# Performance work log

Hardware: AMD Instinct MI355X
Metric: run time of the kernel (lower is better)

Reference implementation:

```python
import jax, jax.numpy as jnp
import numpy as np

N = 100000
E = 1600000
F_IN = 128
F_HID = 128


def gcn_conv(x, src, dst, deg_inv_sqrt, W, b, n_nodes):
    # x: [N, Fin] -> [N, Fout]; symmetric-normalized aggregation with self-loops
    h = x @ W  # [N, Fout]
    norm = deg_inv_sqrt[src] * deg_inv_sqrt[dst]  # [E+N] (self-loops appended)
    msgs = h[src] * norm[:, None]  # [E+N, Fout]
    out = jax.ops.segment_sum(msgs, dst, num_segments=n_nodes)
    return out + b


def setup_inputs() -> dict:
    key = jax.random.key(0)
    k = jax.random.split(key, 8)
    x = jax.random.normal(k[0], (N, F_IN), dtype=jnp.float32)
    edge_index = jax.random.randint(k[1], (2, E), 0, N, dtype=jnp.int32)
    s = 1.0 / np.sqrt(F_IN)
    W1 = jax.random.uniform(k[2], (F_IN, F_HID), jnp.float32, -s, s)
    b1 = jnp.zeros((F_HID,), jnp.float32)
    s2 = 1.0 / np.sqrt(F_HID)
    W2 = jax.random.uniform(k[3], (F_HID, F_HID), jnp.float32, -s2, s2)
    b2 = jnp.zeros((F_HID,), jnp.float32)
    W3 = jax.random.uniform(k[4], (F_HID, 1), jnp.float32, -s2, s2)
    b3 = jnp.zeros((1,), jnp.float32)
    return {"x": x, "edge_index": edge_index, "W1": W1, "b1": b1,
            "W2": W2, "b2": b2, "W3": W3, "b3": b3}


def reference(x, edge_index, W1, b1, W2, b2, W3, b3):
    n = x.shape[0]
    loops = jnp.arange(n, dtype=edge_index.dtype)
    src = jnp.concatenate([edge_index[0], loops])  # add self-loops
    dst = jnp.concatenate([edge_index[1], loops])
    deg = jax.ops.segment_sum(jnp.ones_like(dst, dtype=x.dtype), dst, num_segments=n)
    deg_inv_sqrt = jnp.where(deg > 0, jax.lax.rsqrt(deg), 0.0)

    h = gcn_conv(x, src, dst, deg_inv_sqrt, W1, b1, n)
    h = jax.nn.relu(h)  # dropout is identity at inference
    h = gcn_conv(h, src, dst, deg_inv_sqrt, W2, b2, n)
    h = jax.nn.relu(h)
    h = gcn_conv(h, src, dst, deg_inv_sqrt, W3, b3, n)
    return jax.nn.sigmoid(h)  # [N, 1]
```

## Files before the change

kernel.cpp:

```cpp
#include <hip/hip_runtime.h>
#include <cstdint>
#include <cstddef>

#define NN 100000
#define NE 1600000
#define FD 128
#define NXCD 8
#define RNODES ((NN + NXCD - 1) / NXCD)
#define CAP 208192

typedef int vi4 __attribute__((ext_vector_type(4)));
typedef __attribute__((ext_vector_type(8))) short bf16x8;
typedef __attribute__((ext_vector_type(4))) float f32x4;

__device__ __forceinline__ float bf_lo(uint32_t u) { return __uint_as_float(u << 16); }
__device__ __forceinline__ float bf_hi(uint32_t u) { return __uint_as_float(u & 0xffff0000u); }
__device__ __forceinline__ uint32_t bf_pack(float a, float b) {
    uint32_t ua = __float_as_uint(a), ub = __float_as_uint(b);
    ua += 0x7fffu + ((ua >> 16) & 1u);
    ub += 0x7fffu + ((ub >> 16) & 1u);
    return (ua >> 16) | (ub & 0xffff0000u);
}
__device__ __forceinline__ unsigned short bf1(float a) {
    uint32_t u = __float_as_uint(a);
    u += 0x7fffu + ((u >> 16) & 1u);
    return (unsigned short)(u >> 16);
}

__global__ __launch_bounds__(256) void k_part(const int* __restrict__ src,
                                              const int* __restrict__ dst,
                                              uint32_t* __restrict__ bkt,
                                              int* __restrict__ bcnt, int e) {
    __shared__ int scnt[8];
    __shared__ int sbase[8];
    if (threadIdx.x < 8) scnt[threadIdx.x] = 0;
    __syncthreads();
    const int base = blockIdx.x * 1024 + threadIdx.x * 4;
    const bool valid = base < e;
    int b_[4]; int r_[4]; uint32_t u_[4];
    if (valid) {
        vi4 d4 = __builtin_nontemporal_load((const vi4*)(dst + base));
        vi4 s4 = __builtin_nontemporal_load((const vi4*)(src + base));
        #pragma unroll
        for (int j = 0; j < 4; ++j) {
            int d = d4[j], s = s4[j];
            int b = d / RNODES;
            b_[j] = b;
            u_[j] = ((uint32_t)(d - b * RNODES) << 17) | (uint32_t)s;
            r_[j] = atomicAdd(&scnt[b], 1);
        }
    }
    __syncthreads();
    if (threadIdx.x < 8)
        sbase[threadIdx.x] = atomicAdd(&bcnt[threadIdx.x], scnt[threadIdx.x]);
    __syncthreads();
    if (valid) {
        #pragma unroll
        for (int j = 0; j < 4; ++j) {
            int b = b_[j];
            bkt[(size_t)b * CAP + sbase[b] + r_[j]] = u_[j];
        }
    }
}

__global__ __launch_bounds__(256) void k_hist2(const uint32_t* __restrict__ bkt,
                                               const int* __restrict__ bcnt,
                                               int* __restrict__ cnt) {
    const int xcd  = blockIdx.x & 7;
    const int blk  = blockIdx.x >> 3;
    const int nblk = (int)(gridDim.x >> 3);
    const int m = bcnt[xcd];
    const uint32_t* B = bkt + (size_t)xcd * CAP;
    const int lo = xcd * RNODES;
    for (int i = blk * 256 + threadIdx.x; i < m; i += nblk * 256)
        atomicAdd(&cnt[lo + (int)(B[i] >> 17)], 1);
}

__global__ __launch_bounds__(1024) void k_scan1(const int* __restrict__ cnt,
                                                int* __restrict__ excl,
                                                int* __restrict__ bsum, int n) {
    __shared__ int sh[1024];
    int i = blockIdx.x * 1024 + threadIdx.x;
    int v = (i < n) ? cnt[i] : 0;
    sh[threadIdx.x] = v;
    __syncthreads();
    for (int off = 1; off < 1024; off <<= 1) {
        int t = (threadIdx.x >= off) ? sh[threadIdx.x - off] : 0;
        __syncthreads();
        sh[threadIdx.x] += t;
        __syncthreads();
    }
    if (i < n) excl[i] = sh[threadIdx.x] - v;
    if (threadIdx.x == 1023) bsum[blockIdx.x] = sh[1023];
}

__global__ void k_scan2(int* __restrict__ bsum, int nb) {
    __shared__ int sh[128];
    int t = threadIdx.x;
    int v = (t < nb) ? bsum[t] : 0;
    sh[t] = v;
    __syncthreads();
    for (int off = 1; off < 128; off <<= 1) {
        int u = (t >= off) ? sh[t - off] : 0;
        __syncthreads();
        sh[t] += u;
        __syncthreads();
    }
    if (t < nb) bsum[t] = sh[t] - v;
}

__global__ void k_scan3(int* __restrict__ excl, const int* __restrict__ bsum,
                        int* __restrict__ cursor, const int* __restrict__ cnt,
                        float* __restrict__ dis, int n, int e) {
    int i = blockIdx.x * blockDim.x + threadIdx.x;
    if (i < n) {
        int v = excl[i] + bsum[i >> 10];
        excl[i] = v;
        cursor[i] = v;
        dis[i] = rsqrtf((float)(cnt[i] + 1));
    }
    if (i == 0) excl[n] = e;
}

__global__ __launch_bounds__(256) void k_fill2(const uint32_t* __restrict__ bkt,
                                               const int* __restrict__ bcnt,
                                               int* __restrict__ cursor,
                                               uint2* __restrict__ colw,
                                               const float* __restrict__ dis) {
    const int xcd  = blockIdx.x & 7;
    const int blk  = blockIdx.x >> 3;
    const int nblk = (int)(gridDim.x >> 3);
    const int m = bcnt[xcd];
    const uint32_t* B = bkt + (size_t)xcd * CAP;
    const int lo = xcd * RNODES;
    for (int i = blk * 256 + threadIdx.x; i < m; i += nblk * 256) {
        uint32_t u = B[i];
        int s = (int)(u & 0x1FFFFu);
        int d = lo + (int)(u >> 17);
        int pos = atomicAdd(&cursor[d], 1);
        uint2 cw;
        cw.x = (uint32_t)s;
        cw.y = __float_as_uint(dis[s] * dis[d]);
        colw[pos] = cw;
    }
}

template <typename TIN>
__global__ __launch_bounds__(256) void k_gemm(const TIN* __restrict__ X,
                                              const float* __restrict__ W,
                                              unsigned short* __restrict__ H, int n) {
    __shared__ unsigned short Wl[128][136];
    const int t = threadIdx.x;
    #pragma unroll
    for (int c = 0; c < 16; ++c) {
        int idx4 = (c * 256 + t) * 4;
        int k  = idx4 >> 7;
        int nn = idx4 & 127;
        float4 v = *(const float4*)(W + idx4);
        Wl[nn + 0][k] = bf1(v.x);
        Wl[nn + 1][k] = bf1(v.y);
        Wl[nn + 2][k] = bf1(v.z);
        Wl[nn + 3][k] = bf1(v.w);
    }
    __syncthreads();

    const int wave = t >> 6, lane = t & 63;
    const int row0 = blockIdx.x * 64 + wave * 16;
    if (row0 >= n) return;
    const int arow = row0 + (lane & 15);
    const int kb8  = (lane >> 4) * 8;

    bf16x8 a[4];
    if constexpr (sizeof(TIN) == 4) {
        const float* Xf = (const float*)X;
        #pragma unroll
        for (int kt = 0; kt < 4; ++kt) {
            const float* p = Xf + (size_t)arow * FD + kt * 32 + kb8;
            float4 u0 = *(const float4*)p;
            float4 u1 = *(const float4*)(p + 4);
            bf16x8 f;
            f[0] = (short)bf1(u0.x); f[1] = (short)bf1(u0.y);
            f[2] = (short)bf1(u0.z); f[3] = (short)bf1(u0.w);
            f[4] = (short)bf1(u1.x); f[5] = (short)bf1(u1.y);
            f[6] = (short)bf1(u1.z); f[7] = (short)bf1(u1.w);
            a[kt] = f;
        }
    } else {
        const unsigned short* Xb = (const unsigned short*)X;
        #pragma unroll
        for (int kt = 0; kt < 4; ++kt)
            a[kt] = *(const bf16x8*)(Xb + (size_t)arow * FD + kt * 32 + kb8);
    }

    const int ccol  = lane & 15;
    const int crow0 = row0 + (lane >> 4) * 4;
    #pragma unroll
    for (int nt = 0; nt < 8; ++nt) {
        f32x4 acc = {0.f, 0.f, 0.f, 0.f};
        const int bcol = nt * 16 + (lane & 15);
        #pragma unroll
        for (int kt = 0; kt < 4; ++kt) {
            bf16x8 b = *(const bf16x8*)&Wl[bcol][kt * 32 + kb8];
            acc = __builtin_amdgcn_mfma_f32_16x16x32_bf16(a[kt], b, acc, 0, 0, 0);
        }
        #pragma unroll
        for (int j = 0; j < 4; ++j)
            H[(size_t)(crow0 + j) * FD + nt * 16 + ccol] = bf1(acc[j]);
    }
}

template <int MODE>
__global__ __launch_bounds__(256) void k_agg(const unsigned short* __restrict__ h,
                                             const float* __restrict__ dis,
                                             const int* __restrict__ rp,
                                             const uint2* __restrict__ colw,
                                             const float* __restrict__ bias,
                                             const float* __restrict__ W3,
                                             unsigned short* __restrict__ out,
                                             float* __restrict__ outf, int n) {
    const uint32_t* h32 = (const uint32_t*)h;
    int wid  = (int)((blockIdx.x * (size_t)blockDim.x + threadIdx.x) >> 6);
    int lane = threadIdx.x & 63;
    int w2 = __builtin_amdgcn_readfirstlane(wid);
    int i0 = 2 * w2;
    if (i0 >= n) return;
    int i1 = i0 + 1;
    const bool has1 = (i1 < n);

    const int e00 = rp[i0];
    const int e01 = rp[i0 + 1];
    const int e11 = has1 ? rp[i0 + 2] : e01;

    float di0 = dis[i0];
    float di1 = has1 ? dis[i1] : 0.f;
    float2 acc0, acc1;
    {
        uint32_t su0 = h32[(size_t)i0 * 64 + lane];
        float q0 = di0 * di0;
        acc0.x = bf_lo(su0) * q0; acc0.y = bf_hi(su0) * q0;
        if (has1) {
            uint32_t su1 = h32[(size_t)i1 * 64 + lane];
            float q1 = di1 * di1;
            acc1.x = bf_lo(su1) * q1; acc1.y = bf_hi(su1) * q1;
        } else { acc1.x = acc1.y = 0.f; }
    }

    const int ng0 = (e01 - e00 + 15) >> 4;
    const int ng1 = (e11 - e01 + 15) >> 4;
    const int ng  = ng0 > ng1 ? ng0 : ng1;

    for (int g = 0; g < ng; ++g) {
        const bool do0 = (g < ng0), do1 = (g < ng1);
        int s0[16], s1[16];
        float w0_[16], w1_[16];
        uint32_t v0[16], v1[16];
        if (do0) {
            const int jb = e00 + g * 16;
            if (jb + 16 <= e01) {
                #pragma unroll
                for (int q = 0; q < 16; ++q) {
                    uint2 cw = colw[jb + q];
                    s0[q] = (int)cw.x; w0_[q] = __uint_as_float(cw.y);
                }
            } else {
                #pragma unroll
                for (int q = 0; q < 16; ++q) {
                    int idx = jb + q;
                    int c   = idx < e01 ? idx : e01 - 1;
                    uint2 cw = colw[c];
                    s0[q]  = (int)cw.x;
                    w0_[q] = idx < e01 ? __uint_as_float(cw.y) : 0.f;
                }
            }
        }
        if (do1) {
            const int jb = e01 + g * 16;
            if (jb + 16 <= e11) {
                #pragma unroll
                for (int q = 0; q < 16; ++q) {
                    uint2 cw = colw[jb + q];
                    s1[q] = (int)cw.x; w1_[q] = __uint_as_float(cw.y);
                }
            } else {
                #pragma unroll
                for (int q = 0; q < 16; ++q) {
                    int idx = jb + q;
                    int c   = idx < e11 ? idx : e11 - 1;
                    uint2 cw = colw[c];
                    s1[q]  = (int)cw.x;
                    w1_[q] = idx < e11 ? __uint_as_float(cw.y) : 0.f;
                }
            }
        }
        if (do0) {
            #pragma unroll
            for (int q = 0; q < 16; ++q)
                v0[q] = h32[(size_t)s0[q] * 64 + lane];
        }
        if (do1) {
            #pragma unroll
            for (int q = 0; q < 16; ++q)
                v1[q] = h32[(size_t)s1[q] * 64 + lane];
        }
        if (do0) {
            #pragma unroll
            for (int q = 0; q < 16; ++q) {
                acc0.x = fmaf(w0_[q], bf_lo(v0[q]), acc0.x);
                acc0.y = fmaf(w0_[q], bf_hi(v0[q]), acc0.y);
            }
        }
        if (do1) {
            #pragma unroll
            for (int q = 0; q < 16; ++q) {
                acc1.x = fmaf(w1_[q], bf_lo(v1[q]), acc1.x);
                acc1.y = fmaf(w1_[q], bf_hi(v1[q]), acc1.y);
            }
        }
    }

    float2 b = ((const float2*)bias)[lane];
    acc0.x = fmaxf(acc0.x + b.x, 0.f);
    acc0.y = fmaxf(acc0.y + b.y, 0.f);
    acc1.x = fmaxf(acc1.x + b.x, 0.f);
    acc1.y = fmaxf(acc1.y + b.y, 0.f);

    if (MODE == 0) {
        ((uint32_t*)out)[(size_t)i0 * 64 + lane] = bf_pack(acc0.x, acc0.y);
        if (has1)
            ((uint32_t*)out)[(size_t)i1 * 64 + lane] = bf_pack(acc1.x, acc1.y);
    } else {
        float2 w3 = ((const float2*)W3)[lane];
        float d0 = acc0.x * w3.x + acc0.y * w3.y;
        float d1 = acc1.x * w3.x + acc1.y * w3.y;
        #pragma unroll
        for (int off = 32; off; off >>= 1) {
            d0 += __shfl_xor(d0, off);
            d1 += __shfl_xor(d1, off);
        }
        if (lane == 0) {
            outf[i0] = d0;
            if (has1) outf[i1] = d1;
        }
    }
}

__global__ __launch_bounds__(256) void k_agg1(const float* __restrict__ h3,
                                              const float* __restrict__ dis,
                                              const int* __restrict__ rp,
                                              const uint2* __restrict__ colw,
                                              const float* __restrict__ b3,
                                              float* __restrict__ out, int n) {
    int i    = (int)((blockIdx.x * (size_t)blockDim.x + threadIdx.x) >> 6);
    int lane = threadIdx.x & 63;
    if (i >= n) return;
    float di  = dis[i];
    float acc = (lane == 0) ? di * di * h3[i] : 0.f;
    const int e0 = rp[i], e1 = rp[i + 1];
    for (int base = e0 + lane; base < e1; base += 64) {
        uint2 cw = colw[base];
        acc = fmaf(__uint_as_float(cw.y), h3[(int)cw.x], acc);
    }
    #pragma unroll
    for (int off = 32; off; off >>= 1) acc += __shfl_xor(acc, off);
    if (lane == 0) {
        float v = acc + b3[0];
        out[i] = 1.f / (1.f + expf(-v));
    }
}

static inline size_t alg(size_t x) { return (x + 255) & ~(size_t)255; }

extern "C" void kernel_launch(void* const* d_in, const int* in_sizes, int n_in,
                              void* d_out, int out_size, void* d_ws, size_t ws_size,
                              hipStream_t stream) {
    const float* x   = (const float*)d_in[0];
    const int*   ei  = (const int*)d_in[1];
    const float* W1  = (const float*)d_in[2];
    const float* b1  = (const float*)d_in[3];
    const float* W2  = (const float*)d_in[4];
    const float* b2  = (const float*)d_in[5];
    const float* W3  = (const float*)d_in[6];
    const float* b3  = (const float*)d_in[7];
    float*       out = (float*)d_out;

    const int n = NN, e = NE;
    const int* src = ei;
    const int* dst = ei + e;

    char* w = (char*)d_ws;
    float* dis    = (float*)w;  w += alg((size_t)n * 4);
    int*   cnt    = (int*)w;    w += alg((size_t)n * 4);
    int*   bcnt   = (int*)w;    w += alg((size_t)8 * 4);
    int*   rp     = (int*)w;    w += alg((size_t)(n + 1) * 4);
    int*   cursor = (int*)w;    w += alg((size_t)n * 4);
    int*   bsum   = (int*)w;    w += alg((size_t)128 * 4);
    uint32_t* bkt = (uint32_t*)w; w += alg((size_t)NXCD * CAP * 4);
    uint2* colw   = (uint2*)w;  w += alg((size_t)e * 8);
    unsigned short* bufA = (unsigned short*)w; w += alg((size_t)n * FD * 2);
    unsigned short* bufB = (unsigned short*)w; w += alg((size_t)n * FD * 2);
    float* h3     = (float*)w;  w += alg((size_t)n * 4);

    hipMemsetAsync(cnt, 0, (size_t)n * 4, stream);
    hipMemsetAsync(bcnt, 0, 8 * 4, stream);

    const int B = 256;
    const int gN = (n + B - 1) / B;
    const int nScan = (n + 1023) / 1024;
    const int nChunk = (e + 1023) / 1024;

    k_part<<<nChunk, B, 0, stream>>>(src, dst, bkt, bcnt, e);
    k_hist2<<<2048, B, 0, stream>>>(bkt, bcnt, cnt);
    k_scan1<<<nScan, 1024, 0, stream>>>(cnt, rp, bsum, n);
    k_scan2<<<1, 128, 0, stream>>>(bsum, nScan);
    k_scan3<<<gN, B, 0, stream>>>(rp, bsum, cursor, cnt, dis, n, e);
    k_fill2<<<2048, B, 0, stream>>>(bkt, bcnt, cursor, colw, dis);

    const int gGemm = (n + 63) / 64;
    const int nWave2  = (n + 1) / 2;
    const int gWave2  = (nWave2 * 64 + B - 1) / B;
    const int gWave   = (n * 64 + B - 1) / B;

    k_gemm<float><<<gGemm, B, 0, stream>>>(x, W1, bufA, n);
    k_agg<0><<<gWave2, B, 0, stream>>>(bufA, dis, rp, colw, b1, W3, bufB, h3, n);
    k_gemm<unsigned short><<<gGemm, B, 0, stream>>>(bufB, W2, bufA, n);
    k_agg<1><<<gWave2, B, 0, stream>>>(bufA, dis, rp, colw, b2, W3, bufB, h3, n);
    k_agg1<<<gWave, B, 0, stream>>>(h3, dis, rp, colw, b3, out, n);
}
```

Before: 486.4 us.

## Process four nodes per wave in aggregation and pre-convert weights to bf16

The aggregation kernel now has each 64-lane wave handle four destination nodes instead of two. This issues up to 64 independent gathered row loads per group iteration, raising memory-level parallelism on the edge gather. A small new kernel converts W1 and W2 to bf16 once, so each GEMM block loads bf16 weights instead of converting fp32 per block. The cost is much higher register pressure from the 4x16 index, weight and value arrays, which may lower occupancy or cause spills. Work imbalance also grows, since each wave loops until its highest-degree node is done.

```diff
diff --git a/kernel.cpp b/kernel.cpp
--- a/kernel.cpp
+++ b/kernel.cpp
@@ -25,6 +25,23 @@
     uint32_t u = __float_as_uint(a);
     u += 0x7fffu + ((u >> 16) & 1u);
     return (unsigned short)(u >> 16);
+}
+
+__global__ __launch_bounds__(256) void k_wcvt(const float* __restrict__ W1,
+                                              const float* __restrict__ W2,
+                                              unsigned short* __restrict__ Wb1,
+                                              unsigned short* __restrict__ Wb2) {
+    int idx4 = (blockIdx.x * 256 + threadIdx.x) * 4;
+    if (idx4 < FD * FD) {
+        float4 a = *(const float4*)(W1 + idx4);
+        ushort4 o;
+        o.x = bf1(a.x); o.y = bf1(a.y); o.z = bf1(a.z); o.w = bf1(a.w);
+        *(ushort4*)(Wb1 + idx4) = o;
+        float4 b = *(const float4*)(W2 + idx4);
+        ushort4 p;
+        p.x = bf1(b.x); p.y = bf1(b.y); p.z = bf1(b.z); p.w = bf1(b.w);
+        *(ushort4*)(Wb2 + idx4) = p;
+    }
 }
 
 __global__ __launch_bounds__(256) void k_part(const int* __restrict__ src,
@@ -147,20 +164,21 @@
 
 template <typename TIN>
 __global__ __launch_bounds__(256) void k_gemm(const TIN* __restrict__ X,
-                                              const float* __restrict__ W,
+                                              const unsigned short* __restrict__ Wb,
                                               unsigned short* __restrict__ H, int n) {
     __shared__ unsigned short Wl[128][136];
     const int t = threadIdx.x;
     #pragma unroll
-    for (int c = 0; c < 16; ++c) {
-        int idx4 = (c * 256 + t) * 4;
-        int k  = idx4 >> 7;
-        int nn = idx4 & 127;
-        float4 v = *(const float4*)(W + idx4);
-        Wl[nn + 0][k] = bf1(v.x);
-        Wl[nn + 1][k] = bf1(v.y);
-        Wl[nn + 2][k] = bf1(v.z);
-        Wl[nn + 3][k] = bf1(v.w);
+    for (int c = 0; c < 8; ++c) {
+        int idx8 = (c * 256 + t) * 8;
+        int k  = idx8 >> 7;
+        int nn = idx8 & 127;
+        ushort4 v0 = *(const ushort4*)(Wb + idx8);
+        ushort4 v1 = *(const ushort4*)(Wb + idx8 + 4);
+        Wl[nn + 0][k] = v0.x; Wl[nn + 1][k] = v0.y;
+        Wl[nn + 2][k] = v0.z; Wl[nn + 3][k] = v0.w;
+        Wl[nn + 4][k] = v1.x; Wl[nn + 5][k] = v1.y;
+        Wl[nn + 6][k] = v1.z; Wl[nn + 7][k] = v1.w;
     }
     __syncthreads();
 
@@ -221,125 +239,111 @@
     const uint32_t* h32 = (const uint32_t*)h;
     int wid  = (int)((blockIdx.x * (size_t)blockDim.x + threadIdx.x) >> 6);
     int lane = threadIdx.x & 63;
-    int w2 = __builtin_amdgcn_readfirstlane(wid);
-    int i0 = 2 * w2;
+    int w4 = __builtin_amdgcn_readfirstlane(wid);
+    int i0 = 4 * w4;
     if (i0 >= n) return;
-    int i1 = i0 + 1;
-    const bool has1 = (i1 < n);
-
-    const int e00 = rp[i0];
-    const int e01 = rp[i0 + 1];
-    const int e11 = has1 ? rp[i0 + 2] : e01;
-
-    float di0 = dis[i0];
-    float di1 = has1 ? dis[i1] : 0.f;
-    float2 acc0, acc1;
-    {
-        uint32_t su0 = h32[(size_t)i0 * 64 + lane];
-        float q0 = di0 * di0;
-        acc0.x = bf_lo(su0) * q0; acc0.y = bf_hi(su0) * q0;
-        if (has1) {
-            uint32_t su1 = h32[(size_t)i1 * 64 + lane];
-            float q1 = di1 * di1;
-            acc1.x = bf_lo(su1) * q1; acc1.y = bf_hi(su1) * q1;
-        } else { acc1.x = acc1.y = 0.f; }
-    }
-
-    const int ng0 = (e01 - e00 + 15) >> 4;
-    const int ng1 = (e11 - e01 + 15) >> 4;
-    const int ng  = ng0 > ng1 ? ng0 : ng1;
-
-    for (int g = 0; g < ng; ++g) {
-        const bool do0 = (g < ng0), do1 = (g < ng1);
-        int s0[16], s1[16];
-        float w0_[16], w1_[16];
-        uint32_t v0[16], v1[16];
-        if (do0) {
-            const int jb = e00 + g * 16;
-            if (jb + 16 <= e01) {
+
+    int eb[5];
+    #pragma unroll
+    for (int k = 0; k < 5; ++k) {
+        int idx = i0 + k;
+        eb[k] = rp[idx < n ? idx : n];
+    }
+
+    float2 acc[4];
+    #pragma unroll
+    for (int k = 0; k < 4; ++k) {
+        int i = i0 + k;
+        if (i < n) {
+            float di = dis[i];
+            float q  = di * di;
+            uint32_t su = h32[(size_t)i * 64 + lane];
+            acc[k].x = bf_lo(su) * q;
+            acc[k].y = bf_hi(su) * q;
+        } else { acc[k].x = 0.f; acc[k].y = 0.f; }
+    }
+
+    int ng[4], ngmax = 0;
+    #pragma unroll
+    for (int k = 0; k < 4; ++k) {
+        ng[k] = (eb[k + 1] - eb[k] + 15) >> 4;
+        ngmax = ng[k] > ngmax ? ng[k] : ngmax;
+    }
+
+    for (int g = 0; g < ngmax; ++g) {
+        int s[4][16]; float wt[4][16]; uint32_t v[4][16];
+        #pragma unroll
+        for (int k = 0; k < 4; ++k) {
+            if (g < ng[k]) {
+                const int jb = eb[k] + g * 16;
+                const int ee = eb[k + 1];
+                if (jb + 16 <= ee) {
+                    #pragma unroll
+                    for (int q = 0; q < 16; ++q) {
+                        uint2 cw = colw[jb + q];
+                        s[k][q] = (int)cw.x; wt[k][q] = __uint_as_float(cw.y);
+                    }
+                } else {
+                    #pragma unroll
+                    for (int q = 0; q < 16; ++q) {
+                        int idx = jb + q;
+                        int c   = idx < ee ? idx : ee - 1;
+                        uint2 cw = colw[c];
+                        s[k][q]  = (int)cw.x;
+                        wt[k][q] = idx < ee ? __uint_as_float(cw.y) : 0.f;
+                    }
+                }
+            }
+        }
+        #pragma unroll
+        for (int k = 0; k < 4; ++k) {
+            if (g < ng[k]) {
+                #pragma unroll
+                for (int q = 0; q < 16; ++q)
+                    v[k][q] = h32[(size_t)s[k][q] * 64 + lane];
+            }
+        }
+        #pragma unroll
+        for (int k = 0; k < 4; ++k) {
+            if (g < ng[k]) {
                 #pragma unroll
                 for (int q = 0; q < 16; ++q) {
-                    uint2 cw = colw[jb + q];
-                    s0[q] = (int)cw.x; w0_[q] = __uint_as_float(cw.y);
-                }
-            } else {
-                #pragma unroll
-                for (int q = 0; q < 16; ++q) {
-                    int idx = jb + q;
-                    int c   = idx < e01 ? idx : e01 - 1;
-                    uint2 cw = colw[c];
-                    s0[q]  = (int)cw.x;
-                    w0_[q] = idx < e01 ? __uint_as_float(cw.y) : 0.f;
+                    acc[k].x = fmaf(wt[k][q], bf_lo(v[k][q]), acc[k].x);
+                    acc[k].y = fmaf(wt[k][q], bf_hi(v[k][q]), acc[k].y);
                 }
             }
         }
-        if (do1) {
-            const int jb = e01 + g * 16;
-            if (jb + 16 <= e11) {
-                #pragma unroll
-                for (int q = 0; q < 16; ++q) {
-                    uint2 cw = colw[jb + q];
-                    s1[q] = (int)cw.x; w1_[q] = __uint_as_float(cw.y);
-                }
-            } else {
-                #pragma unroll
-                for (int q = 0; q < 16; ++q) {
-                    int idx = jb + q;
-                    int c   = idx < e11 ? idx : e11 - 1;
-                    uint2 cw = colw[c];
-                    s1[q]  = (int)cw.x;
-                    w1_[q] = idx < e11 ? __uint_as_float(cw.y) : 0.f;
-                }
-            }
-        }
-        if (do0) {
-            #pragma unroll
-            for (int q = 0; q < 16; ++q)
-                v0[q] = h32[(size_t)s0[q] * 64 + lane];
-        }
-        if (do1) {
-            #pragma unroll
-            for (int q = 0; q < 16; ++q)
-                v1[q] = h32[(size_t)s1[q] * 64 + lane];
-        }
-        if (do0) {
-            #pragma unroll
-            for (int q = 0; q < 16; ++q) {
-                acc0.x = fmaf(w0_[q], bf_lo(v0[q]), acc0.x);
-                acc0.y = fmaf(w0_[q], bf_hi(v0[q]), acc0.y);
-            }
-        }
-        if (do1) {
-            #pragma unroll
-            for (int q = 0; q < 16; ++q) {
-                acc1.x = fmaf(w1_[q], bf_lo(v1[q]), acc1.x);
-                acc1.y = fmaf(w1_[q], bf_hi(v1[q]), acc1.y);
-            }
-        }
     }
 
     float2 b = ((const float2*)bias)[lane];
-    acc0.x = fmaxf(acc0.x + b.x, 0.f);
-    acc0.y = fmaxf(acc0.y + b.y, 0.f);
-    acc1.x = fmaxf(acc1.x + b.x, 0.f);
-    acc1.y = fmaxf(acc1.y + b.y, 0.f);
+    #pragma unroll
+    for (int k = 0; k < 4; ++k) {
+        acc[k].x = fmaxf(acc[k].x + b.x, 0.f);
+        acc[k].y = fmaxf(acc[k].y + b.y, 0.f);
+    }
 
     if (MODE == 0) {
-        ((uint32_t*)out)[(size_t)i0 * 64 + lane] = bf_pack(acc0.x, acc0.y);
-        if (has1)
-            ((uint32_t*)out)[(size_t)i1 * 64 + lane] = bf_pack(acc1.x, acc1.y);
+        #pragma unroll
+        for (int k = 0; k < 4; ++k) {
+            if (i0 + k < n)
+                ((uint32_t*)out)[(size_t)(i0 + k) * 64 + lane] =
+                    bf_pack(acc[k].x, acc[k].y);
+        }
     } else {
         float2 w3 = ((const float2*)W3)[lane];
-        float d0 = acc0.x * w3.x + acc0.y * w3.y;
-        float d1 = acc1.x * w3.x + acc1.y * w3.y;
+        float d[4];
+        #pragma unroll
+        for (int k = 0; k < 4; ++k)
+            d[k] = acc[k].x * w3.x + acc[k].y * w3.y;
         #pragma unroll
         for (int off = 32; off; off >>= 1) {
-            d0 += __shfl_xor(d0, off);
-            d1 += __shfl_xor(d1, off);
+            #pragma unroll
+            for (int k = 0; k < 4; ++k) d[k] += __shfl_xor(d[k], off);
         }
         if (lane == 0) {
-            outf[i0] = d0;
-            if (has1) outf[i1] = d1;
+            #pragma unroll
+            for (int k = 0; k < 4; ++k)
+                if (i0 + k < n) outf[i0 + k] = d[k];
         }
     }
 }
@@ -398,6 +402,8 @@
     uint2* colw   = (uint2*)w;  w += alg((size_t)e * 8);
     unsigned short* bufA = (unsigned short*)w; w += alg((size_t)n * FD * 2);
     unsigned short* bufB = (unsigned short*)w; w += alg((size_t)n * FD * 2);
+    unsigned short* Wb1  = (unsigned short*)w; w += alg((size_t)FD * FD * 2);
+    unsigned short* Wb2  = (unsigned short*)w; w += alg((size_t)FD * FD * 2);
     float* h3     = (float*)w;  w += alg((size_t)n * 4);
 
     hipMemsetAsync(cnt, 0, (size_t)n * 4, stream);
@@ -408,6 +414,7 @@
     const int nScan = (n + 1023) / 1024;
     const int nChunk = (e + 1023) / 1024;
 
+    k_wcvt<<<16, B, 0, stream>>>(W1, W2, Wb1, Wb2);
     k_part<<<nChunk, B, 0, stream>>>(src, dst, bkt, bcnt, e);
     k_hist2<<<2048, B, 0, stream>>>(bkt, bcnt, cnt);
     k_scan1<<<nScan, 1024, 0, stream>>>(cnt, rp, bsum, n);
@@ -416,13 +423,13 @@
     k_fill2<<<2048, B, 0, stream>>>(bkt, bcnt, cursor, colw, dis);
 
     const int gGemm = (n + 63) / 64;
-    const int nWave2  = (n + 1) / 2;
-    const int gWave2  = (nWave2 * 64 + B - 1) / B;
-    const int gWave   = (n * 64 + B - 1) / B;
-
-    k_gemm<float><<<gGemm, B, 0, stream>>>(x, W1, bufA, n);
-    k_agg<0><<<gWave2, B, 0, stream>>>(bufA, dis, rp, colw, b1, W3, bufB, h3, n);
-    k_gemm<unsigned short><<<gGemm, B, 0, stream>>>(bufB, W2, bufA, n);
-    k_agg<1><<<gWave2, B, 0, stream>>>(bufA, dis, rp, colw, b2, W3, bufB, h3, n);
+    const int nWave4 = (n + 3) / 4;
+    const int gWave4 = (nWave4 * 64 + B - 1) / B;
+    const int gWave  = (n * 64 + B - 1) / B;
+
+    k_gemm<float><<<gGemm, B, 0, stream>>>(x, Wb1, bufA, n);
+    k_agg<0><<<gWave4, B, 0, stream>>>(bufA, dis, rp, colw, b1, W3, bufB, h3, n);
+    k_gemm<unsigned short><<<gGemm, B, 0, stream>>>(bufB, Wb2, bufA, n);
+    k_agg<1><<<gWave4, B, 0, stream>>>(bufA, dis, rp, colw, b2, W3, bufB, h3, n);
     k_agg1<<<gWave, B, 0, stream>>>(h3, dis, rp, colw, b3, out, n);
 }
```

After: 543.6 us. 1.12x slower.
